# Kernel tuning notes

Measured on AMD Instinct MI355X. Metric: run time of the kernel, lower is better.

The kernel has to match this reference:

```python
import jax, jax.numpy as jnp
import numpy as np

D_MODEL = 128; D_STATE = 64; D_CONV = 4; EXPAND = 2; HEADDIM = 32; NGROUPS = 1
D_INNER = EXPAND * D_MODEL            # 256
NHEADS = D_INNER // HEADDIM           # 8
CONV_DIM = D_INNER + 2 * NGROUPS * D_STATE   # 384 (x, B, C streams)
D_IN_PROJ = 2 * D_INNER + 2 * NGROUPS * D_STATE + NHEADS  # 648 (z, xBC, dt)
EPS = 1e-5


def setup_inputs() -> dict:
    key = jax.random.key(0)
    ks = jax.random.split(key, 8)
    B, L = 8, 4096
    x = jax.random.normal(ks[0], (B, L, D_MODEL), jnp.float32)
    norm_w = jnp.ones((D_MODEL,), jnp.float32)
    in_proj_w = jax.random.normal(ks[1], (D_IN_PROJ, D_MODEL), jnp.float32) * (D_MODEL ** -0.5)
    conv_w = jax.random.normal(ks[2], (CONV_DIM, D_CONV), jnp.float32) * (D_CONV ** -0.5)
    conv_b = jnp.zeros((CONV_DIM,), jnp.float32)
    dt_bias = jax.random.uniform(ks[3], (NHEADS,), jnp.float32, -4.0, -1.0)
    A_log = jnp.log(jax.random.uniform(ks[4], (NHEADS,), jnp.float32, 1.0, 16.0))
    D = jnp.ones((NHEADS,), jnp.float32)
    gnorm_w = jnp.ones((D_INNER,), jnp.float32)
    out_proj_w = jax.random.normal(ks[5], (D_MODEL, D_INNER), jnp.float32) * (D_INNER ** -0.5)
    return dict(x=x, norm_w=norm_w, in_proj_w=in_proj_w, conv_w=conv_w, conv_b=conv_b,
                dt_bias=dt_bias, A_log=A_log, D=D, gnorm_w=gnorm_w, out_proj_w=out_proj_w)


def _rmsnorm(x, w):
    return x * jax.lax.rsqrt(jnp.mean(x * x, axis=-1, keepdims=True) + EPS) * w


def _causal_dw_conv(x, w, b):
    # x: [B,L,C]; w: [C,K]; depthwise causal conv along L
    K = w.shape[1]
    xp = jnp.pad(x, ((0, 0), (K - 1, 0), (0, 0)))
    kern = jnp.transpose(w)[:, None, :]  # [K,1,C] for WIO with groups=C
    out = jax.lax.conv_general_dilated(
        xp, kern, window_strides=(1,), padding='VALID',
        dimension_numbers=('NWC', 'WIO', 'NWC'),
        feature_group_count=w.shape[0])
    return out + b


def _ssm(xh, dt, Bm, Cm, A):
    # xh: [B,L,H,P]; dt: [B,L,H]; Bm, Cm: [B,L,N]; A: [H]
    def step(h, inp):
        x_t, dt_t, B_t, C_t = inp
        dA = jnp.exp(dt_t * A)                                   # [B,H]
        h = h * dA[..., None, None] + (dt_t[..., None] * x_t)[..., None] * B_t[:, None, None, :]
        y = jnp.einsum('bhpn,bn->bhp', h, C_t)
        return h, y
    Bsz, L, H, P = xh.shape
    N = Bm.shape[-1]
    h0 = jnp.zeros((Bsz, H, P, N), xh.dtype)
    xs = (xh.transpose(1, 0, 2, 3), dt.transpose(1, 0, 2),
          Bm.transpose(1, 0, 2), Cm.transpose(1, 0, 2))
    _, ys = jax.lax.scan(step, h0, xs)
    return ys.transpose(1, 0, 2, 3)  # [B,L,H,P]


def reference(x, norm_w, in_proj_w, conv_w, conv_b, dt_bias, A_log, D, gnorm_w, out_proj_w):
    xn = _rmsnorm(x, norm_w)
    zxbcdt = xn @ in_proj_w.T                                    # [B,L,648]
    z, xBC, dt = jnp.split(zxbcdt, [D_INNER, D_INNER + CONV_DIM], axis=-1)
    dt = jax.nn.softplus(dt + dt_bias)                           # [B,L,H]
    xBC = jax.nn.silu(_causal_dw_conv(xBC, conv_w, conv_b))
    xs, Bm, Cm = jnp.split(xBC, [D_INNER, D_INNER + NGROUPS * D_STATE], axis=-1)
    Bsz, L, _ = x.shape
    xh = xs.reshape(Bsz, L, NHEADS, HEADDIM)
    A = -jnp.exp(A_log)                                          # [H]
    y = _ssm(xh, dt, Bm, Cm, A) + D[None, None, :, None] * xh    # D skip per head
    y = y.reshape(Bsz, L, D_INNER)
    y = _rmsnorm(y * jax.nn.silu(z), gnorm_w)                    # gated RMSNorm
    out = y @ out_proj_w.T
    return x + out
```

## Files before the change

### kernel.cpp

```cpp
#include <hip/hip_runtime.h>

#define DM    128
#define DI    256
#define NH    8
#define HD    32
#define NS    64
#define CDIM  384
#define DPROJ 648
#define LSEQ  4096
#define NB    8
#define NTOK  32768
#define LC    64
#define NC    64
#define EPSF  1e-5f
#define LOG2E 1.4426950408889634f

typedef __bf16 bf16;
typedef bf16  bf16x8 __attribute__((ext_vector_type(8)));
typedef bf16  bf16x4 __attribute__((ext_vector_type(4)));
typedef short short8 __attribute__((ext_vector_type(8)));
typedef float f32x4  __attribute__((ext_vector_type(4)));

__device__ __forceinline__ unsigned short f2bfbits(float f) {
    unsigned int u = __float_as_uint(f);
    unsigned int r = u + 0x7FFFu + ((u >> 16) & 1u);
    return (unsigned short)(r >> 16);
}
__device__ __forceinline__ float bfbits2f(unsigned short u) {
    return __uint_as_float(((unsigned int)u) << 16);
}

__global__ __launch_bounds__(256) void k_prep(const float* __restrict__ w1,
                                              const float* __restrict__ w2,
                                              const float* __restrict__ gw,
                                              unsigned short* __restrict__ w1g,
                                              unsigned short* __restrict__ w2f) {
    int i = blockIdx.x * 256 + threadIdx.x;
    if (i < 640 * DM) {
        int f = i >> 9, r = i & 511;
        int lane = r >> 3, jj = r & 7;
        int ns = f >> 2, kk = f & 3;
        int n = ns * 16 + (lane & 15), k = kk * 32 + (lane >> 4) * 8 + jj;
        w1g[i] = f2bfbits(w1[(size_t)n * DM + k]);
    } else {
        int j = i - 640 * DM;
        if (j < DM * DI) {
            int f = j >> 9, r = j & 511;
            int lane = r >> 3, jj = r & 7;
            int kk = f >> 3, nt = f & 7;
            int fr = lane & 15, ko = lane >> 4;
            int n = nt * 16 + fr, k = kk * 32 + ko * 8 + jj;
            w2f[j] = f2bfbits(w2[(size_t)n * DI + k] * gw[k]);
        }
    }
}

__global__ __launch_bounds__(512) void k_front(const float* __restrict__ x,
                                               const float* __restrict__ nw,
                                               const float* __restrict__ w1,
                                               const float* __restrict__ dtb,
                                               const unsigned short* __restrict__ w1g,
                                               const float* __restrict__ cw,
                                               const float* __restrict__ cb,
                                               const float* __restrict__ alog,
                                               unsigned short* __restrict__ zb,
                                               float* __restrict__ dtf,
                                               unsigned short* __restrict__ bcA,
                                               unsigned short* __restrict__ xT,
                                               unsigned short* __restrict__ hst,
                                               float* __restrict__ dAp) {
    __shared__ __align__(16) unsigned char SMEM[117120];
    unsigned short* XBC = (unsigned short*)SMEM;
    float*          Xs  = (float*)(SMEM + 62720);
    unsigned short* Lc  = (unsigned short*)(SMEM + 62720);
    float*          Wd  = (float*)(SMEM + 108800);
    float*          dts = (float*)(SMEM + 113024);
    float*          wlh = (float*)(SMEM + 115072);
    const int tid = threadIdx.x;
    const int wave = tid >> 6, lane = tid & 63;
    const int t0 = blockIdx.x * 64;
    const int l0 = t0 & (LSEQ - 1);
    if (tid < 256) {
        int row = tid >> 5, col = (tid & 31) * 4;
        *(float4*)&Wd[row * 132 + col] = *(const float4*)(w1 + (size_t)(640 + row) * DM + col);
    }
    const float nw0 = nw[lane * 2], nw1 = nw[lane * 2 + 1];
    #pragma unroll
    for (int i = 0; i < 10; i++) {
        int r = wave * 10 + i;
        int tok = t0 + r - 16; if (tok < 0) tok = 0;
        const float* xr = x + (size_t)tok * DM + lane * 2;
        float v0 = xr[0], v1 = xr[1];
        float ss = v0 * v0 + v1 * v1;
        #pragma unroll
        for (int o = 32; o; o >>= 1) ss += __shfl_xor(ss, o);
        float rs = rsqrtf(ss * (1.0f / DM) + EPSF);
        Xs[r * 132 + lane * 2]     = v0 * rs * nw0;
        Xs[r * 132 + lane * 2 + 1] = v1 * rs * nw1;
    }
    __syncthreads();
    {
        const int h = lane >> 3, ks = lane & 7;
        const float dtbh = dtb[h];
        #pragma unroll
        for (int i = 0; i < 8; i++) {
            int rw = wave * 8 + i;
            int r = 16 + rw;
            float acc = 0.f;
            #pragma unroll
            for (int q = 0; q < 4; q++) {
                float4 xv = *(const float4*)&Xs[r * 132 + ks * 16 + q * 4];
                float4 wv = *(const float4*)&Wd[h * 132 + ks * 16 + q * 4];
                acc = fmaf(xv.x, wv.x, acc); acc = fmaf(xv.y, wv.y, acc);
                acc = fmaf(xv.z, wv.z, acc); acc = fmaf(xv.w, wv.w, acc);
            }
            acc += __shfl_xor(acc, 1);
            acc += __shfl_xor(acc, 2);
            acc += __shfl_xor(acc, 4);
            if (ks == 0) {
                float v = acc + dtbh;
                float sp = (v > 20.f) ? v : log1pf(expf(v));
                dtf[(size_t)(t0 + rw) * NH + h] = sp;
                dts[rw * NH + h] = sp;
            }
        }
    }
    const int wm = wave >> 2, wn = wave & 3;
    const int fr = lane & 15, ko = lane >> 4;
    bf16x8 a0[4], a1[4], ah[4];
    #pragma unroll
    for (int kk = 0; kk < 4; kk++) {
        const float* s0 = &Xs[(16 + wm * 32 + fr) * 132 + kk * 32 + ko * 8];
        const float* s1 = &Xs[(16 + wm * 32 + 16 + fr) * 132 + kk * 32 + ko * 8];
        const float* sh = &Xs[fr * 132 + kk * 32 + ko * 8];
        bf16x8 f0, f1, fh;
        #pragma unroll
        for (int j = 0; j < 8; j++) {
            f0[j] = (bf16)s0[j]; f1[j] = (bf16)s1[j]; fh[j] = (bf16)sh[j];
        }
        a0[kk] = f0; a1[kk] = f1; ah[kk] = fh;
    }
    for (int i = 0; i < 10; i++) {
        int f = i * 4 + wn;
        const unsigned short* wb = w1g + (((size_t)f * 4) << 9) + lane * 8;
        f32x4 acc0 = {}, acc1 = {}, accH = {};
        #pragma unroll
        for (int kk = 0; kk < 4; kk++) {
            bf16x8 bfr = *(const bf16x8*)(wb + ((size_t)kk << 9));
            acc0 = __builtin_amdgcn_mfma_f32_16x16x32_bf16(a0[kk], bfr, acc0, 0, 0, 0);
            acc1 = __builtin_amdgcn_mfma_f32_16x16x32_bf16(a1[kk], bfr, acc1, 0, 0, 0);
            if (i >= 4 && wm == 0)
                accH = __builtin_amdgcn_mfma_f32_16x16x32_bf16(ah[kk], bfr, accH, 0, 0, 0);
        }
        if (i < 4) {
            int n = f * 16 + fr;
            #pragma unroll
            for (int rr = 0; rr < 4; rr++) {
                zb[(size_t)(t0 + wm * 32 + ko * 4 + rr) * DI + n]      = f2bfbits(acc0[rr]);
                zb[(size_t)(t0 + wm * 32 + 16 + ko * 4 + rr) * DI + n] = f2bfbits(acc1[rr]);
            }
        } else {
            int cc = f * 16 + fr - 256;
            #pragma unroll
            for (int rr = 0; rr < 4; rr++) {
                XBC[(16 + wm * 32 + ko * 4 + rr) * 392 + cc]      = f2bfbits(acc0[rr]);
                XBC[(16 + wm * 32 + 16 + ko * 4 + rr) * 392 + cc] = f2bfbits(acc1[rr]);
            }
            if (wm == 0) {
                #pragma unroll
                for (int rr = 0; rr < 4; rr++)
                    XBC[(ko * 4 + rr) * 392 + cc] = f2bfbits(accH[rr]);
            }
        }
    }
    __syncthreads();
    if (tid < CDIM) {
        const int ch = tid;
        float4 wv = *(const float4*)(cw + ch * 4);
        float bias = cb[ch];
        float h1 = 0.f, h2 = 0.f, h3 = 0.f;
        if (l0) {
            h1 = bfbits2f(XBC[15 * 392 + ch]);
            h2 = bfbits2f(XBC[14 * 392 + ch]);
            h3 = bfbits2f(XBC[13 * 392 + ch]);
        }
        short8 pk;
        #pragma unroll 8
        for (int t = 0; t < 64; t++) {
            float x0 = bfbits2f(XBC[(16 + t) * 392 + ch]);
            float acc = bias;
            acc = fmaf(x0, wv.w, acc);
            acc = fmaf(h1, wv.z, acc);
            acc = fmaf(h2, wv.y, acc);
            acc = fmaf(h3, wv.x, acc);
            float s = acc / (1.f + expf(-acc));
            unsigned short us = f2bfbits(s);
            if (ch >= 256) bcA[(size_t)(t0 + t) * 128 + (ch - 256)] = us;
            pk[t & 7] = (short)us;
            if (ch < 320 && (t & 7) == 7) *(short8*)&Lc[ch * 72 + t - 7] = pk;
            h3 = h2; h2 = h1; h1 = x0;
        }
    }
    __syncthreads();
    {
        int idx = tid;
        #pragma unroll
        for (int it = 0; it < 4; it++, idx += 512) {
            int row = idx >> 3, tc = (idx & 7) * 8;
            *(short8*)(xT + (size_t)row * NTOK + t0 + tc) = *(const short8*)&Lc[row * 72 + tc];
        }
    }
    {
        const int h = wave;
        const int b = blockIdx.x >> 6, c = blockIdx.x & 63;
        const int bh = b * NH + h;
        const float A = -expf(alog[h]);
        float dt = dts[lane * NH + h];
        float q = dt * A * LOG2E;
        #pragma unroll
        for (int o = 1; o <= 32; o <<= 1) {
            float tmp = __shfl_up(q, o);
            if (lane >= o) q += tmp;
        }
        float qL = __shfl(q, 63);
        wlh[h * 64 + lane] = exp2f(qL - q) * dt;
        if (lane == 0) dAp[(size_t)bh * NC + c] = exp2f(qL);
        const int m = lane & 15;
        f32x4 hacc[4][2] = {};
        #pragma unroll
        for (int kh = 0; kh < 2; kh++) {
            bf16x8 xb[2];
            #pragma unroll
            for (int pi = 0; pi < 2; pi++)
                xb[pi] = *(const bf16x8*)&Lc[(h * HD + pi * 16 + m) * 72 + kh * 32 + ko * 8];
            f32x4 w0 = *(const f32x4*)&wlh[h * 64 + kh * 32 + ko * 8];
            f32x4 w1v = *(const f32x4*)&wlh[h * 64 + kh * 32 + ko * 8 + 4];
            #pragma unroll
            for (int ni = 0; ni < 4; ni++) {
                bf16x8 bv = *(const bf16x8*)&Lc[(256 + ni * 16 + m) * 72 + kh * 32 + ko * 8];
                bf16x8 af;
                #pragma unroll
                for (int j = 0; j < 4; j++) af[j] = (bf16)((float)bv[j] * w0[j]);
                #pragma unroll
                for (int j = 0; j < 4; j++) af[4 + j] = (bf16)((float)bv[4 + j] * w1v[j]);
                #pragma unroll
                for (int pi = 0; pi < 2; pi++)
                    hacc[ni][pi] = __builtin_amdgcn_mfma_f32_16x16x32_bf16(af, xb[pi], hacc[ni][pi], 0, 0, 0);
            }
        }
        unsigned short* hb = hst + (((size_t)bh * NC + c) << 11);
        #pragma unroll
        for (int ni = 0; ni < 4; ni++)
            #pragma unroll
            for (int pi = 0; pi < 2; pi++) {
                bf16x4 pv;
                #pragma unroll
                for (int r = 0; r < 4; r++) pv[r] = (bf16)hacc[ni][pi][r];
                *(bf16x4*)(hb + (pi * 16 + m) * 64 + ni * 16 + ko * 4) = pv;
            }
    }
}

__global__ __launch_bounds__(256) void k_ssm2(unsigned short* __restrict__ hst,
                                              const float* __restrict__ dAp) {
    __shared__ float dl[NC];
    const int bh = blockIdx.x >> 3, seg = blockIdx.x & 7;
    const int s = seg * 256 + threadIdx.x;
    if (threadIdx.x < NC) dl[threadIdx.x] = dAp[(size_t)bh * NC + threadIdx.x];
    __syncthreads();
    unsigned short* p = hst + ((size_t)bh * NC << 11) + s;
    float r = 0.f;
    float v0 = bfbits2f(p[0]);
    float v1 = bfbits2f(p[(size_t)1 << 11]);
    float v2 = bfbits2f(p[(size_t)2 << 11]);
    float v3 = bfbits2f(p[(size_t)3 << 11]);
    for (int c = 0; c < NC; c += 4) {
        float t;
        t = v0; if (c + 4 < NC) v0 = bfbits2f(p[(size_t)(c + 4) << 11]);
        p[(size_t)c << 11] = f2bfbits(r);       r = fmaf(r, dl[c], t);
        t = v1; if (c + 5 < NC) v1 = bfbits2f(p[(size_t)(c + 5) << 11]);
        p[(size_t)(c + 1) << 11] = f2bfbits(r); r = fmaf(r, dl[c + 1], t);
        t = v2; if (c + 6 < NC) v2 = bfbits2f(p[(size_t)(c + 6) << 11]);
        p[(size_t)(c + 2) << 11] = f2bfbits(r); r = fmaf(r, dl[c + 2], t);
        t = v3; if (c + 7 < NC) v3 = bfbits2f(p[(size_t)(c + 7) << 11]);
        p[(size_t)(c + 3) << 11] = f2bfbits(r); r = fmaf(r, dl[c + 3], t);
    }
}

__global__ __launch_bounds__(512, 2) void k_ssd3g(const unsigned short* __restrict__ bcA,
                                                  const unsigned short* __restrict__ xT,
                                                  const float* __restrict__ dtf,
                                                  const float* __restrict__ alog,
                                                  const unsigned short* __restrict__ hst,
                                                  const float* __restrict__ Dw,
                                                  const unsigned short* __restrict__ zb,
                                                  const unsigned short* __restrict__ w2f,
                                                  const float* __restrict__ xin,
                                                  float* __restrict__ out) {
    __shared__ __align__(16) unsigned short BC[64][136];
    __shared__ __align__(16) bf16 PlY[NH][64 * 40];
    __shared__ float ql[NH][64];
    __shared__ float dl[NH][64];
    const int tid = threadIdx.x;
    const int b = blockIdx.x >> 6, c = blockIdx.x & 63;
    const int t0 = blockIdx.x * 64;
    const size_t tok0 = (size_t)t0;
    {
        int idx = tid;
        #pragma unroll
        for (int it = 0; it < 2; it++, idx += 512) {
            int tok = idx >> 4, c8 = (idx & 15) * 8;
            *(short8*)&BC[tok][c8] = *(const short8*)(bcA + (tok0 + tok) * 128 + c8);
        }
    }
    __syncthreads();
    const int h = tid >> 6, lane = tid & 63;
    const int bh = b * NH + h;
    const float A = -expf(alog[h]);
    const float Dh = Dw[h];
    float dt = dtf[(tok0 + lane) * NH + h];
    float q = dt * A * LOG2E;
    #pragma unroll
    for (int o = 1; o <= 32; o <<= 1) {
        float tmp = __shfl_up(q, o);
        if (lane >= o) q += tmp;
    }
    ql[h][lane] = q;
    dl[h][lane] = dt;
    const int m = lane & 15, ko = lane >> 4;
    bf16* Pw = &PlY[h][0];
    bf16x8 cf[4][2];
    #pragma unroll
    for (int ti = 0; ti < 4; ti++)
        #pragma unroll
        for (int kh = 0; kh < 2; kh++)
            cf[ti][kh] = *(const bf16x8*)&BC[ti * 16 + m][64 + kh * 32 + ko * 8];
    float qt[4];
    #pragma unroll
    for (int ti = 0; ti < 4; ti++) qt[ti] = ql[h][ti * 16 + m];
    const size_t hbase = ((size_t)bh * NC + c) << 11;
    f32x4 ya[4][2] = {}, ua[4][2] = {};
    #pragma unroll
    for (int kh = 0; kh < 2; kh++) {
        bf16x8 hb2[2];
        #pragma unroll
        for (int pi = 0; pi < 2; pi++)
            hb2[pi] = *(const bf16x8*)(hst + hbase + (pi * 16 + m) * 64 + kh * 32 + ko * 8);
        #pragma unroll
        for (int ti = 0; ti < 4; ti++)
            #pragma unroll
            for (int pi = 0; pi < 2; pi++)
                ua[ti][pi] = __builtin_amdgcn_mfma_f32_16x16x32_bf16(cf[ti][kh], hb2[pi], ua[ti][pi], 0, 0, 0);
    }
    #pragma unroll
    for (int sh = 0; sh < 2; sh++) {
        f32x4 gth[4][2] = {};
        #pragma unroll
        for (int kh = 0; kh < 2; kh++) {
            bf16x8 bfg[2];
            #pragma unroll
            for (int sj = 0; sj < 2; sj++)
                bfg[sj] = *(const bf16x8*)&BC[(sh * 2 + sj) * 16 + m][kh * 32 + ko * 8];
            #pragma unroll
            for (int ti = 0; ti < 4; ti++)
                #pragma unroll
                for (int sj = 0; sj < 2; sj++)
                    gth[ti][sj] = __builtin_amdgcn_mfma_f32_16x16x32_bf16(bfg[sj], cf[ti][kh], gth[ti][sj], 0, 0, 0);
        }
        #pragma unroll
        for (int sj = 0; sj < 2; sj++) {
            const int si = sh * 2 + sj;
            f32x4 qs = *(const f32x4*)&ql[h][si * 16 + ko * 4];
            f32x4 ds = *(const f32x4*)&dl[h][si * 16 + ko * 4];
            #pragma unroll
            for (int ti = 0; ti < 4; ti++) {
                bf16x4 pv = {};
                if (si <= ti) {
                    const int t = ti * 16 + m;
                    #pragma unroll
                    for (int r = 0; r < 4; r++) {
                        int s = si * 16 + ko * 4 + r;
                        float p = 0.f;
                        if (s <= t) {
                            p = exp2f(qt[ti] - qs[r]) * ds[r] * gth[ti][sj][r];
                            if (s == t) p += Dh;
                        }
                        pv[r] = (bf16)p;
                    }
                }
                *(bf16x4*)&Pw[(ti * 16 + m) * 40 + sj * 16 + ko * 4] = pv;
            }
        }
        bf16x8 xb[2];
        #pragma unroll
        for (int pi = 0; pi < 2; pi++)
            xb[pi] = *(const bf16x8*)(xT + (size_t)(h * HD + pi * 16 + m) * NTOK + tok0 + sh * 32 + ko * 8);
        #pragma unroll
        for (int ti = 0; ti < 4; ti++) {
            bf16x8 pa = *(const bf16x8*)&Pw[(ti * 16 + m) * 40 + ko * 8];
            #pragma unroll
            for (int pi = 0; pi < 2; pi++)
                ya[ti][pi] = __builtin_amdgcn_mfma_f32_16x16x32_bf16(pa, xb[pi], ya[ti][pi], 0, 0, 0);
        }
    }
    __syncthreads();
    unsigned short* Ys = (unsigned short*)&PlY[0][0];
    {
        f32x4 et[4];
        #pragma unroll
        for (int ti = 0; ti < 4; ti++) {
            f32x4 qv = *(const f32x4*)&ql[h][ti * 16 + ko * 4];
            #pragma unroll
            for (int r = 0; r < 4; r++) et[ti][r] = exp2f(qv[r]);
        }
        #pragma unroll
        for (int ti = 0; ti < 4; ti++)
            #pragma unroll
            for (int pi = 0; pi < 2; pi++)
                #pragma unroll
                for (int r = 0; r < 4; r++) {
                    int t = ti * 16 + ko * 4 + r;
                    Ys[t * 264 + h * HD + pi * 16 + m] =
                        f2bfbits(ya[ti][pi][r] + et[ti][r] * ua[ti][pi][r]);
                }
    }
    __syncthreads();
    {
        const int rg = h & 3, nh = h >> 2;
        const int r0 = rg * 16;
        const size_t rowo = (tok0 + r0 + m) * DI;
        float ss = 0.f;
        bf16x8 gb[8];
        #pragma unroll
        for (int kk = 0; kk < 8; kk++) {
            int co = kk * 32 + ko * 8;
            bf16x8 yv = *(const bf16x8*)&Ys[(r0 + m) * 264 + co];
            bf16x8 zv = *(const bf16x8*)(zb + rowo + co);
            #pragma unroll
            for (int j = 0; j < 8; j++) {
                float z = (float)zv[j];
                float g = (float)yv[j] * (z / (1.f + expf(-z)));
                ss += g * g;
                gb[kk][j] = (bf16)g;
            }
        }
        ss += __shfl_xor(ss, 16);
        ss += __shfl_xor(ss, 32);
        const float rs = rsqrtf(ss * (1.0f / DI) + EPSF);
        #pragma unroll
        for (int kk = 0; kk < 8; kk++)
            #pragma unroll
            for (int j = 0; j < 8; j++)
                gb[kk][j] = (bf16)((float)gb[kk][j] * rs);
        const unsigned short* wp = w2f + (size_t)lane * 8;
        f32x4 acc[4] = {};
        #pragma unroll
        for (int kk = 0; kk < 8; kk++) {
            #pragma unroll
            for (int ntl = 0; ntl < 4; ntl++) {
                bf16x8 bfr = *(const bf16x8*)(wp + (((size_t)kk * 8 + nh * 4 + ntl) << 9));
                acc[ntl] = __builtin_amdgcn_mfma_f32_16x16x32_bf16(gb[kk], bfr, acc[ntl], 0, 0, 0);
            }
        }
        #pragma unroll
        for (int ntl = 0; ntl < 4; ntl++) {
            int n = (nh * 4 + ntl) * 16 + m;
            #pragma unroll
            for (int rr = 0; rr < 4; rr++) {
                size_t row = tok0 + r0 + ko * 4 + rr;
                out[row * DM + n] = xin[row * DM + n] + acc[ntl][rr];
            }
        }
    }
}

extern "C" void kernel_launch(void* const* d_in, const int* in_sizes, int n_in,
                              void* d_out, int out_size, void* d_ws, size_t ws_size,
                              hipStream_t stream) {
    const float* x   = (const float*)d_in[0];
    const float* nw  = (const float*)d_in[1];
    const float* w1  = (const float*)d_in[2];
    const float* cw  = (const float*)d_in[3];
    const float* cb  = (const float*)d_in[4];
    const float* dtb = (const float*)d_in[5];
    const float* al  = (const float*)d_in[6];
    const float* Dw  = (const float*)d_in[7];
    const float* gw  = (const float*)d_in[8];
    const float* w2  = (const float*)d_in[9];
    float* out = (float*)d_out;

    float* ws = (float*)d_ws;
    float*  dAp = ws;
    float*  dtf = dAp + NB * NH * NC;
    unsigned short* hst = (unsigned short*)(dtf + (size_t)NTOK * NH);
    unsigned short* zb  = hst + (size_t)NB * NH * NC * 2048;
    unsigned short* bcA = zb + (size_t)NTOK * DI;
    unsigned short* xT  = bcA + (size_t)NTOK * 128;
    unsigned short* w1g = xT + (size_t)DI * NTOK;
    unsigned short* w2f = w1g + (size_t)640 * DM;

    k_prep<<<(640 * DM + DM * DI + 255) / 256, 256, 0, stream>>>(w1, w2, gw, w1g, w2f);
    k_front<<<NTOK / 64, 512, 0, stream>>>(x, nw, w1, dtb, w1g, cw, cb, al,
                                           zb, dtf, bcA, xT, hst, dAp);
    k_ssm2<<<NB * NH * 8, 256, 0, stream>>>(hst, dAp);
    k_ssd3g<<<NTOK / 64, 512, 0, stream>>>(bcA, xT, dtf, al, hst, Dw, zb, w2f, x, out);
}
```

Baseline: 180.2 us.

## Shrink k_front shared memory with channel-major bf16 xBC tile and in-place conv

Reorganizes k_front's shared memory from about 117KB to 64KB. The projected xBC is now stored channel-major in bf16, with halo rows written into a small per-channel slot. The depthwise conv then reads and writes 8-wide vectors in place, and later stages reuse that same buffer, which removes the separate Lc transpose copy. The goal is to fit more blocks per CU (launch bounds 512,4) and vectorize LDS traffic. The cost is an extra barrier and aliasing of Xs with XT.

```diff
diff --git a/kernel.cpp b/kernel.cpp
--- a/kernel.cpp
+++ b/kernel.cpp
@@ -55,27 +55,27 @@
     }
 }
 
-__global__ __launch_bounds__(512) void k_front(const float* __restrict__ x,
-                                               const float* __restrict__ nw,
-                                               const float* __restrict__ w1,
-                                               const float* __restrict__ dtb,
-                                               const unsigned short* __restrict__ w1g,
-                                               const float* __restrict__ cw,
-                                               const float* __restrict__ cb,
-                                               const float* __restrict__ alog,
-                                               unsigned short* __restrict__ zb,
-                                               float* __restrict__ dtf,
-                                               unsigned short* __restrict__ bcA,
-                                               unsigned short* __restrict__ xT,
-                                               unsigned short* __restrict__ hst,
-                                               float* __restrict__ dAp) {
-    __shared__ __align__(16) unsigned char SMEM[117120];
-    unsigned short* XBC = (unsigned short*)SMEM;
-    float*          Xs  = (float*)(SMEM + 62720);
-    unsigned short* Lc  = (unsigned short*)(SMEM + 62720);
-    float*          Wd  = (float*)(SMEM + 108800);
-    float*          dts = (float*)(SMEM + 113024);
-    float*          wlh = (float*)(SMEM + 115072);
+__global__ __launch_bounds__(512, 4) void k_front(const float* __restrict__ x,
+                                                  const float* __restrict__ nw,
+                                                  const float* __restrict__ w1,
+                                                  const float* __restrict__ dtb,
+                                                  const unsigned short* __restrict__ w1g,
+                                                  const float* __restrict__ cw,
+                                                  const float* __restrict__ cb,
+                                                  const float* __restrict__ alog,
+                                                  unsigned short* __restrict__ zb,
+                                                  float* __restrict__ dtf,
+                                                  unsigned short* __restrict__ bcA,
+                                                  unsigned short* __restrict__ xTg,
+                                                  unsigned short* __restrict__ hst,
+                                                  float* __restrict__ dAp) {
+    __shared__ __align__(16) unsigned char SMEM[65536];
+    float*          Xs  = (float*)SMEM;
+    unsigned short* XT  = (unsigned short*)SMEM;
+    unsigned short* Hb  = (unsigned short*)(SMEM + 33792);
+    float*          Wd  = (float*)(SMEM + 38144);
+    float*          dts = (float*)(SMEM + 61440);
+    float*          wlh = (float*)(SMEM + 63488);
     const int tid = threadIdx.x;
     const int wave = tid >> 6, lane = tid & 63;
     const int t0 = blockIdx.x * 64;
@@ -95,8 +95,14 @@
         #pragma unroll
         for (int o = 32; o; o >>= 1) ss += __shfl_xor(ss, o);
         float rs = rsqrtf(ss * (1.0f / DM) + EPSF);
-        Xs[r * 132 + lane * 2]     = v0 * rs * nw0;
-        Xs[r * 132 + lane * 2 + 1] = v1 * rs * nw1;
+        float o0 = v0 * rs * nw0, o1 = v1 * rs * nw1;
+        if (r < 16) {
+            ushort2 hb; hb.x = f2bfbits(o0); hb.y = f2bfbits(o1);
+            *(ushort2*)&Hb[r * 136 + lane * 2] = hb;
+        } else {
+            Xs[(r - 16) * 132 + lane * 2]     = o0;
+            Xs[(r - 16) * 132 + lane * 2 + 1] = o1;
+        }
     }
     __syncthreads();
     {
@@ -105,11 +111,10 @@
         #pragma unroll
         for (int i = 0; i < 8; i++) {
             int rw = wave * 8 + i;
-            int r = 16 + rw;
             float acc = 0.f;
             #pragma unroll
             for (int q = 0; q < 4; q++) {
-                float4 xv = *(const float4*)&Xs[r * 132 + ks * 16 + q * 4];
+                float4 xv = *(const float4*)&Xs[rw * 132 + ks * 16 + q * 4];
                 float4 wv = *(const float4*)&Wd[h * 132 + ks * 16 + q * 4];
                 acc = fmaf(xv.x, wv.x, acc); acc = fmaf(xv.y, wv.y, acc);
                 acc = fmaf(xv.z, wv.z, acc); acc = fmaf(xv.w, wv.w, acc);
@@ -130,16 +135,15 @@
     bf16x8 a0[4], a1[4], ah[4];
     #pragma unroll
     for (int kk = 0; kk < 4; kk++) {
-        const float* s0 = &Xs[(16 + wm * 32 + fr) * 132 + kk * 32 + ko * 8];
-        const float* s1 = &Xs[(16 + wm * 32 + 16 + fr) * 132 + kk * 32 + ko * 8];
-        const float* sh = &Xs[fr * 132 + kk * 32 + ko * 8];
-        bf16x8 f0, f1, fh;
-        #pragma unroll
-        for (int j = 0; j < 8; j++) {
-            f0[j] = (bf16)s0[j]; f1[j] = (bf16)s1[j]; fh[j] = (bf16)sh[j];
-        }
-        a0[kk] = f0; a1[kk] = f1; ah[kk] = fh;
-    }
+        const float* s0 = &Xs[(wm * 32 + fr) * 132 + kk * 32 + ko * 8];
+        const float* s1 = &Xs[(wm * 32 + 16 + fr) * 132 + kk * 32 + ko * 8];
+        bf16x8 f0, f1;
+        #pragma unroll
+        for (int j = 0; j < 8; j++) { f0[j] = (bf16)s0[j]; f1[j] = (bf16)s1[j]; }
+        a0[kk] = f0; a1[kk] = f1;
+        ah[kk] = *(const bf16x8*)&Hb[fr * 136 + kk * 32 + ko * 8];
+    }
+    __syncthreads();
     for (int i = 0; i < 10; i++) {
         int f = i * 4 + wn;
         const unsigned short* wb = w1g + (((size_t)f * 4) << 9) + lane * 8;
@@ -161,15 +165,16 @@
             }
         } else {
             int cc = f * 16 + fr - 256;
-            #pragma unroll
-            for (int rr = 0; rr < 4; rr++) {
-                XBC[(16 + wm * 32 + ko * 4 + rr) * 392 + cc]      = f2bfbits(acc0[rr]);
-                XBC[(16 + wm * 32 + 16 + ko * 4 + rr) * 392 + cc] = f2bfbits(acc1[rr]);
-            }
-            if (wm == 0) {
-                #pragma unroll
-                for (int rr = 0; rr < 4; rr++)
-                    XBC[(ko * 4 + rr) * 392 + cc] = f2bfbits(accH[rr]);
+            bf16x4 p0, p1;
+            #pragma unroll
+            for (int rr = 0; rr < 4; rr++) { p0[rr] = (bf16)acc0[rr]; p1[rr] = (bf16)acc1[rr]; }
+            *(bf16x4*)&XT[cc * 80 + 8 + wm * 32 + ko * 4]      = p0;
+            *(bf16x4*)&XT[cc * 80 + 8 + wm * 32 + 16 + ko * 4] = p1;
+            if (wm == 0 && ko == 3) {
+                bf16x4 pH;
+                #pragma unroll
+                for (int rr = 0; rr < 4; rr++) pH[rr] = (bf16)accH[rr];
+                *(bf16x4*)&XT[cc * 80 + 4] = pH;
             }
         }
     }
@@ -178,27 +183,27 @@
         const int ch = tid;
         float4 wv = *(const float4*)(cw + ch * 4);
         float bias = cb[ch];
+        bf16x4 hv = *(const bf16x4*)&XT[ch * 80 + 4];
         float h1 = 0.f, h2 = 0.f, h3 = 0.f;
-        if (l0) {
-            h1 = bfbits2f(XBC[15 * 392 + ch]);
-            h2 = bfbits2f(XBC[14 * 392 + ch]);
-            h3 = bfbits2f(XBC[13 * 392 + ch]);
-        }
-        short8 pk;
-        #pragma unroll 8
-        for (int t = 0; t < 64; t++) {
-            float x0 = bfbits2f(XBC[(16 + t) * 392 + ch]);
-            float acc = bias;
-            acc = fmaf(x0, wv.w, acc);
-            acc = fmaf(h1, wv.z, acc);
-            acc = fmaf(h2, wv.y, acc);
-            acc = fmaf(h3, wv.x, acc);
-            float s = acc / (1.f + expf(-acc));
-            unsigned short us = f2bfbits(s);
-            if (ch >= 256) bcA[(size_t)(t0 + t) * 128 + (ch - 256)] = us;
-            pk[t & 7] = (short)us;
-            if (ch < 320 && (t & 7) == 7) *(short8*)&Lc[ch * 72 + t - 7] = pk;
-            h3 = h2; h2 = h1; h1 = x0;
+        if (l0) { h1 = (float)hv[3]; h2 = (float)hv[2]; h3 = (float)hv[1]; }
+        #pragma unroll
+        for (int u = 0; u < 8; u++) {
+            bf16x8 iv = *(const bf16x8*)&XT[ch * 80 + 8 + u * 8];
+            bf16x8 ov;
+            #pragma unroll
+            for (int j = 0; j < 8; j++) {
+                float x0 = (float)iv[j];
+                float acc = bias;
+                acc = fmaf(x0, wv.w, acc);
+                acc = fmaf(h1, wv.z, acc);
+                acc = fmaf(h2, wv.y, acc);
+                acc = fmaf(h3, wv.x, acc);
+                float s = acc / (1.f + expf(-acc));
+                ov[j] = (bf16)s;
+                if (ch >= 256) bcA[(size_t)(t0 + u * 8 + j) * 128 + (ch - 256)] = f2bfbits(s);
+                h3 = h2; h2 = h1; h1 = x0;
+            }
+            *(bf16x8*)&XT[ch * 80 + 8 + u * 8] = ov;
         }
     }
     __syncthreads();
@@ -207,7 +212,7 @@
         #pragma unroll
         for (int it = 0; it < 4; it++, idx += 512) {
             int row = idx >> 3, tc = (idx & 7) * 8;
-            *(short8*)(xT + (size_t)row * NTOK + t0 + tc) = *(const short8*)&Lc[row * 72 + tc];
+            *(short8*)(xTg + (size_t)row * NTOK + t0 + tc) = *(const short8*)&XT[row * 80 + 8 + tc];
         }
     }
     {
@@ -232,12 +237,12 @@
             bf16x8 xb[2];
             #pragma unroll
             for (int pi = 0; pi < 2; pi++)
-                xb[pi] = *(const bf16x8*)&Lc[(h * HD + pi * 16 + m) * 72 + kh * 32 + ko * 8];
+                xb[pi] = *(const bf16x8*)&XT[(h * HD + pi * 16 + m) * 80 + 8 + kh * 32 + ko * 8];
             f32x4 w0 = *(const f32x4*)&wlh[h * 64 + kh * 32 + ko * 8];
             f32x4 w1v = *(const f32x4*)&wlh[h * 64 + kh * 32 + ko * 8 + 4];
             #pragma unroll
             for (int ni = 0; ni < 4; ni++) {
-                bf16x8 bv = *(const bf16x8*)&Lc[(256 + ni * 16 + m) * 72 + kh * 32 + ko * 8];
+                bf16x8 bv = *(const bf16x8*)&XT[(256 + ni * 16 + m) * 80 + 8 + kh * 32 + ko * 8];
                 bf16x8 af;
                 #pragma unroll
                 for (int j = 0; j < 4; j++) af[j] = (bf16)((float)bv[j] * w0[j]);
```

Result: faster. 165.2 us (-8.3%).
